# Performance work log

Measured on AMD Instinct MI355X. Metric: run time of the kernel, lower is better.

Reference implementation:

```python
import jax, jax.numpy as jnp
import numpy as np

EMBED_DIM = 1024
NUM_HEADS = 16
HEAD_DIM = EMBED_DIM // NUM_HEADS  # 64
B, NQ, NK = 4, 1024, 2048


def setup_inputs() -> dict:
    key = jax.random.key(0)
    ks = jax.random.split(key, 13)
    s = 1.0 / np.sqrt(EMBED_DIM)
    inp = {
        "query": jax.random.normal(ks[0], (B, NQ, EMBED_DIM), jnp.float32),
        "key": jax.random.normal(ks[1], (B, NK, EMBED_DIM), jnp.float32),
        "value": jax.random.normal(ks[2], (B, NK, EMBED_DIM), jnp.float32),
        # positive multiplicity weights per key element
        "key_multiplicities": jax.random.uniform(ks[3], (B, NK), jnp.float32, 0.1, 4.0),
        "wq_w": jax.random.normal(ks[4], (EMBED_DIM, EMBED_DIM), jnp.float32) * s,
        "wq_b": jnp.zeros((EMBED_DIM,), jnp.float32),
        "wk_w": jax.random.normal(ks[5], (EMBED_DIM, EMBED_DIM), jnp.float32) * s,
        "wk_b": jnp.zeros((EMBED_DIM,), jnp.float32),
        "wv_w": jax.random.normal(ks[6], (EMBED_DIM, EMBED_DIM), jnp.float32) * s,
        "wv_b": jnp.zeros((EMBED_DIM,), jnp.float32),
        "wo_w": jax.random.normal(ks[7], (EMBED_DIM, EMBED_DIM), jnp.float32) * s,
        "wo_b": jnp.zeros((EMBED_DIM,), jnp.float32),
    }
    return inp


def _split_heads(x, b, n):
    # (b, n, h*d) -> (b, h, n, d)
    return x.reshape(b, n, NUM_HEADS, HEAD_DIM).transpose(0, 2, 1, 3)


def reference(query, key, value, key_multiplicities,
              wq_w, wq_b, wk_w, wk_b, wv_w, wv_b, wo_w, wo_b):
    b, n_q, _ = query.shape
    _, n_k, _ = key.shape
    q = _split_heads(query @ wq_w.T + wq_b, b, n_q)   # (b, h, n_q, d)
    k = _split_heads(key @ wk_w.T + wk_b, b, n_k)     # (b, h, n_k, d)
    v = _split_heads(value @ wv_w.T + wv_b, b, n_k)   # (b, h, n_k, d)
    scale = 1.0 / jnp.sqrt(jnp.asarray(HEAD_DIM, q.dtype))
    scores = jnp.einsum("bhqd,bhkd->bhqk", q, k) * scale
    # multiplicities weight each key: softmax_i(m_i * exp(s_i)) == softmax(s_i + log m_i)
    logits = scores + jnp.log(key_multiplicities)[:, None, None, :]
    attn = jax.nn.softmax(logits, axis=-1)            # (b, h, n_q, n_k)
    out = jnp.einsum("bhqk,bhkd->bhqd", attn, v)
    out = out.transpose(0, 2, 1, 3).reshape(b, n_q, NUM_HEADS * HEAD_DIM)
    return out @ wo_w.T + wo_b
```

## Files before the change

kernel.cpp:

```cpp
#include <hip/hip_runtime.h>
#include <hip/hip_bf16.h>
#include <stdint.h>
#include <stddef.h>

typedef __attribute__((ext_vector_type(8))) short bf16x8;
typedef __attribute__((ext_vector_type(4))) short short4v;
typedef __attribute__((ext_vector_type(4))) float f32x4;
typedef __attribute__((ext_vector_type(2))) uint32_t u32x2;
typedef __attribute__((ext_vector_type(4))) uint32_t u32x4;

#define MFMA16(a, b, c) __builtin_amdgcn_mfma_f32_16x16x32_bf16((a), (b), (c), 0, 0, 0)

__device__ __forceinline__ short f2bf(float f) {
    uint32_t u = __builtin_bit_cast(uint32_t, f);
    u = (u + 0x7FFFu + ((u >> 16) & 1u)) >> 16;
    return (short)(uint16_t)u;
}

__device__ __forceinline__ uint32_t pkbf(float a, float b) {
#if __has_builtin(__builtin_amdgcn_cvt_pk_bf16_f32)
    auto r = __builtin_amdgcn_cvt_pk_bf16_f32(a, b);
    return __builtin_bit_cast(uint32_t, r);
#else
    return (uint32_t)(uint16_t)f2bf(a) | ((uint32_t)(uint16_t)f2bf(b) << 16);
#endif
}

__device__ __forceinline__ float fexp2(float x) {
#if __has_builtin(__builtin_amdgcn_exp2f)
    return __builtin_amdgcn_exp2f(x);
#else
    return exp2f(x);
#endif
}

__device__ __forceinline__ void gload16(const short* g, short* l) {
    __builtin_amdgcn_global_load_lds(
        (const __attribute__((address_space(1))) unsigned int*)g,
        (__attribute__((address_space(3))) unsigned int*)l, 16, 0, 0);
}

__global__ __launch_bounds__(256) void prep_kernel(
        const float* __restrict__ w0, const float* __restrict__ w1,
        const float* __restrict__ w2, const float* __restrict__ w3,
        const float* __restrict__ q, const float* __restrict__ k,
        const float* __restrict__ v, const float* __restrict__ m,
        short* __restrict__ wb, short* __restrict__ Qa,
        short* __restrict__ Ka, short* __restrict__ Va,
        float* __restrict__ lm) {
    const int bid = blockIdx.x;
    if (bid >= 12288) {
        const int i = ((bid - 12288) * 256 + threadIdx.x) * 8;
        f32x4 a = *(const f32x4*)(m + i);
        f32x4 b = *(const f32x4*)(m + i + 4);
        f32x4 oa, ob;
        #pragma unroll
        for (int j = 0; j < 4; ++j) { oa[j] = __log2f(a[j]); ob[j] = __log2f(b[j]); }
        *(f32x4*)(lm + i) = oa;
        *(f32x4*)(lm + i + 4) = ob;
        return;
    }
    const float* src;
    short* dst;
    int local;
    if (bid < 2048) {
        const int z = bid >> 9;
        local = bid & 511;
        src = (z == 0) ? w0 : (z == 1) ? w1 : (z == 2) ? w2 : w3;
        dst = wb + (size_t)z * 1048576;
    } else if (bid < 4096) { src = q; dst = Qa; local = bid - 2048; }
    else if (bid < 8192)   { src = k; dst = Ka; local = bid - 4096; }
    else                   { src = v; dst = Va; local = bid - 8192; }
    const size_t i = ((size_t)local * 256 + threadIdx.x) * 8;
    f32x4 a = *(const f32x4*)(src + i);
    f32x4 b = *(const f32x4*)(src + i + 4);
    u32x4 o = { pkbf(a[0], a[1]), pkbf(a[2], a[3]), pkbf(b[0], b[1]), pkbf(b[2], b[3]) };
    *(u32x4*)(dst + i) = o;
}

__global__ __launch_bounds__(256) void proj_kernel(
        const short* __restrict__ Qa, const short* __restrict__ Ka,
        const short* __restrict__ Va, const short* __restrict__ wb,
        const float* __restrict__ wq_b, const float* __restrict__ wk_b,
        const float* __restrict__ wv_b, short* __restrict__ Qp,
        short* __restrict__ Kp, short* __restrict__ Vt, const int ybase) {
    __shared__ short As[128 * 32];
    __shared__ short Bs[128 * 32];

    const int cpx = gridDim.x >> 3;
    const int l = (blockIdx.x & 7) * cpx + (blockIdx.x >> 3);
    const int y = (l >> 3) + ybase;
    const int tn = (l & 7) * 128;

    const short* A; const short* W; const float* bias; int mode, tm;
    if (y < 32)      { A = Qa; W = wb;           bias = wq_b; mode = 0; tm = y * 128; }
    else if (y < 96) { A = Ka; W = wb + 1048576; bias = wk_b; mode = 1; tm = (y - 32) * 128; }
    else             { A = Va; W = wb + 2097152; bias = wv_b; mode = 2; tm = (y - 96) * 128; }

    const int t = threadIdx.x, lane = t & 63, w = t >> 6;
    const int wr = w >> 1, wc = w & 1;
    const int qd = lane >> 4, c = lane & 15;

    f32x4 acc[4][4];
    #pragma unroll
    for (int i = 0; i < 4; ++i)
        #pragma unroll
        for (int j = 0; j < 4; ++j) acc[i][j] = (f32x4){0.f, 0.f, 0.f, 0.f};

    const int r0 = w * 16 + (lane >> 2);
    const int qc = (lane & 3) ^ ((lane >> 3) & 3);
    const short* ga0 = A + (size_t)(tm + r0) * 1024 + qc * 8;
    const short* ga1 = ga0 + 64 * 1024;
    const short* gb0 = W + (size_t)(tn + r0) * 1024 + qc * 8;
    const short* gb1 = gb0 + 64 * 1024;
    short* la0 = &As[w * 512];
    short* la1 = &As[w * 512 + 2048];
    short* lb0 = &Bs[w * 512];
    short* lb1 = &Bs[w * 512 + 2048];
    const int swz = (qd ^ ((c >> 1) & 3)) * 8;

    for (int k0 = 0; k0 < 1024; k0 += 32) {
        __syncthreads();
        gload16(ga0 + k0, la0);
        gload16(ga1 + k0, la1);
        gload16(gb0 + k0, lb0);
        gload16(gb1 + k0, lb1);
        __syncthreads();
        bf16x8 af[4], bfr[4];
        #pragma unroll
        for (int rt = 0; rt < 4; ++rt)
            af[rt] = *(const bf16x8*)&As[(wr * 64 + rt * 16 + c) * 32 + swz];
        #pragma unroll
        for (int ct = 0; ct < 4; ++ct)
            bfr[ct] = *(const bf16x8*)&Bs[(wc * 64 + ct * 16 + c) * 32 + swz];
        #pragma unroll
        for (int rt = 0; rt < 4; ++rt)
            #pragma unroll
            for (int ct = 0; ct < 4; ++ct)
                acc[rt][ct] = MFMA16(af[rt], bfr[ct], acc[rt][ct]);
    }

    float bv[4];
    #pragma unroll
    for (int ct = 0; ct < 4; ++ct) bv[ct] = bias[tn + wc * 64 + ct * 16 + c];

    if (mode == 2) {
        #pragma unroll
        for (int rt = 0; rt < 4; ++rt)
            #pragma unroll
            for (int ct = 0; ct < 4; ++ct) {
                const int cg = tn + wc * 64 + ct * 16 + c;
                const int h = cg >> 6, d = cg & 63;
                const int rg0 = tm + wr * 64 + rt * 16 + qd * 4;
                const int bb = rg0 >> 11, n = rg0 & 2047;
                u32x2 pk = { pkbf(acc[rt][ct][0] + bv[ct], acc[rt][ct][1] + bv[ct]),
                             pkbf(acc[rt][ct][2] + bv[ct], acc[rt][ct][3] + bv[ct]) };
                *(u32x2*)&Vt[((((size_t)(bb * 16 + h)) * 64 + d) << 11) + n] = pk;
            }
    } else {
        short* out = (mode == 0) ? Qp : Kp;
        const int nshift = (mode == 0) ? 10 : 11;
        const int mask = (1 << nshift) - 1;
        #pragma unroll
        for (int rt = 0; rt < 4; ++rt)
            #pragma unroll
            for (int ct = 0; ct < 4; ++ct) {
                const int cg = tn + wc * 64 + ct * 16 + c;
                const int h = cg >> 6, d = cg & 63;
                #pragma unroll
                for (int r = 0; r < 4; ++r) {
                    const int rg = tm + wr * 64 + rt * 16 + qd * 4 + r;
                    const int bb = rg >> nshift, n = rg & mask;
                    out[((((size_t)(bb * 16 + h)) << nshift) + n) * 64 + d] =
                        f2bf(acc[rt][ct][r] + bv[ct]);
                }
            }
    }
}

__global__ __launch_bounds__(256, 4) void gemm_o_kernel(
        const short* __restrict__ Ob, const short* __restrict__ W,
        const float* __restrict__ bias, float* __restrict__ out) {
    __shared__ short As[128 * 32];
    __shared__ short Bs[64 * 32];

    const int cpx = gridDim.x >> 3;
    const int l = (blockIdx.x & 7) * cpx + (blockIdx.x >> 3);
    const int tm = (l >> 4) * 128, tn = (l & 15) * 64;

    const int t = threadIdx.x, lane = t & 63, w = t >> 6;
    const int wr = w >> 1, wc = w & 1;
    const int qd = lane >> 4, c = lane & 15;

    f32x4 acc[4][2];
    #pragma unroll
    for (int i = 0; i < 4; ++i)
        #pragma unroll
        for (int j = 0; j < 2; ++j) acc[i][j] = (f32x4){0.f, 0.f, 0.f, 0.f};

    const int r0 = w * 16 + (lane >> 2);
    const int qc = (lane & 3) ^ ((lane >> 3) & 3);
    const short* ga0 = Ob + (size_t)(tm + r0) * 1024 + qc * 8;
    const short* ga1 = ga0 + 64 * 1024;
    const short* gb0 = W + (size_t)(tn + r0) * 1024 + qc * 8;
    short* la0 = &As[w * 512];
    short* la1 = &As[w * 512 + 2048];
    short* lb0 = &Bs[w * 512];
    const int swz = (qd ^ ((c >> 1) & 3)) * 8;

    for (int k0 = 0; k0 < 1024; k0 += 32) {
        __syncthreads();
        gload16(ga0 + k0, la0);
        gload16(ga1 + k0, la1);
        gload16(gb0 + k0, lb0);
        __syncthreads();
        bf16x8 af[4], bfr[2];
        #pragma unroll
        for (int rt = 0; rt < 4; ++rt)
            af[rt] = *(const bf16x8*)&As[(wr * 64 + rt * 16 + c) * 32 + swz];
        #pragma unroll
        for (int ct = 0; ct < 2; ++ct)
            bfr[ct] = *(const bf16x8*)&Bs[(wc * 32 + ct * 16 + c) * 32 + swz];
        #pragma unroll
        for (int rt = 0; rt < 4; ++rt)
            #pragma unroll
            for (int ct = 0; ct < 2; ++ct)
                acc[rt][ct] = MFMA16(af[rt], bfr[ct], acc[rt][ct]);
    }

    float bv[2];
    #pragma unroll
    for (int ct = 0; ct < 2; ++ct) bv[ct] = bias[tn + wc * 32 + ct * 16 + c];

    #pragma unroll
    for (int rt = 0; rt < 4; ++rt)
        #pragma unroll
        for (int ct = 0; ct < 2; ++ct) {
            const int cg = tn + wc * 32 + ct * 16 + c;
            #pragma unroll
            for (int r = 0; r < 4; ++r) {
                const int rg = tm + wr * 64 + rt * 16 + qd * 4 + r;
                out[(size_t)rg * 1024 + cg] = acc[rt][ct][r] + bv[ct];
            }
        }
}

__global__ __launch_bounds__(256, 2) void attn_kernel(
        const short* __restrict__ Qp, const short* __restrict__ Kp,
        const short* __restrict__ Vt, const float* __restrict__ logm,
        short* __restrict__ Ob) {
    __shared__ short Ps[128 * 128];
    __shared__ short Vs[64 * 128];
    __shared__ float Lm[128];
    short* Ks = Ps;

    const int bid = blockIdx.x;
    const int xcd = bid & 7, ii = bid >> 3;
    const int qt = ii >> 3, bh = xcd + ((ii & 7) << 3);
    const int b = bh >> 4;
    const int t = threadIdx.x, lane = t & 63, w = t >> 6;
    const int qd = lane >> 4, c = lane & 15;
    const int cl = c & 7;
    const float SC = 0.18033688011112042f;

    bf16x8 qf[2][2];
    #pragma unroll
    for (int ct = 0; ct < 2; ++ct)
        #pragma unroll
        for (int kd = 0; kd < 2; ++kd)
            qf[ct][kd] = *(const bf16x8*)(Qp +
                ((size_t)bh * 1024 + qt * 128 + w * 32 + ct * 16 + c) * 64 + kd * 32 + qd * 8);

    bf16x8 onesf;
    {
        const short ov = (c == 0) ? (short)0x3F80 : (short)0;
        #pragma unroll
        for (int j = 0; j < 8; ++j) onesf[j] = ov;
    }

    f32x4 oacc[2][5];
    #pragma unroll
    for (int i = 0; i < 2; ++i)
        #pragma unroll
        for (int j = 0; j < 5; ++j) oacc[i][j] = (f32x4){0.f, 0.f, 0.f, 0.f};

    const short* kgp[4];
    short* klp[4];
    const short* vgp[4];
    short* vlp[4];
    {
        const int krow = lane >> 3;
        const int kchk = (lane & 7) ^ krow;
        const int vrow = lane >> 4;
        #pragma unroll
        for (int i = 0; i < 4; ++i) {
            const int rk = w * 32 + i * 8 + krow;
            kgp[i] = Kp + ((size_t)bh * 2048 + rk) * 64 + kchk * 8;
            klp[i] = &Ks[(w * 4 + i) * 512];
            const int rv = w * 16 + i * 4 + vrow;
            const int vchk = (lane & 15) ^ (rv & 7);
            vgp[i] = Vt + ((size_t)bh * 64 + rv) * 2048 + vchk * 8;
            vlp[i] = &Vs[(w * 4 + i) * 512];
        }
    }

    for (int kt = 0; kt < 16; ++kt) {
        #pragma unroll
        for (int i = 0; i < 4; ++i) {
            gload16(kgp[i] + (size_t)kt * 8192, klp[i]);
            gload16(vgp[i] + kt * 128, vlp[i]);
        }
        if (t < 128) Lm[t] = logm[b * 2048 + kt * 128 + t];
        __syncthreads();

        f32x4 s[8][2];
        #pragma unroll
        for (int rt = 0; rt < 8; ++rt) {
            bf16x8 a0 = *(const bf16x8*)&Ks[(rt * 16 + c) * 64 + (qd ^ cl) * 8];
            bf16x8 a1 = *(const bf16x8*)&Ks[(rt * 16 + c) * 64 + ((4 | qd) ^ cl) * 8];
            #pragma unroll
            for (int ct = 0; ct < 2; ++ct) {
                f32x4 z = (f32x4){0.f, 0.f, 0.f, 0.f};
                s[rt][ct] = MFMA16(a1, qf[ct][1], MFMA16(a0, qf[ct][0], z));
            }
        }
        __syncthreads();

        #pragma unroll
        for (int rt = 0; rt < 8; ++rt) {
            f32x4 lv = *(const f32x4*)&Lm[rt * 16 + qd * 4];
            #pragma unroll
            for (int ct = 0; ct < 2; ++ct) {
                float p0 = fexp2(__builtin_fmaf(s[rt][ct][0], SC, lv[0]));
                float p1 = fexp2(__builtin_fmaf(s[rt][ct][1], SC, lv[1]));
                float p2 = fexp2(__builtin_fmaf(s[rt][ct][2], SC, lv[2]));
                float p3 = fexp2(__builtin_fmaf(s[rt][ct][3], SC, lv[3]));
                u32x2 pk = { pkbf(p0, p1), pkbf(p2, p3) };
                const int prow = w * 32 + ct * 16 + c;
                const int pch = (2 * rt + (qd >> 1)) ^ cl;
                *(u32x2*)&Ps[prow * 128 + pch * 8 + (qd & 1) * 4] = pk;
            }
        }

        #pragma unroll
        for (int kk = 0; kk < 4; ++kk) {
            const int lch = ((kk * 4 + qd) ^ cl) * 8;
            bf16x8 pf[2], vf[4];
            #pragma unroll
            for (int rtq = 0; rtq < 2; ++rtq)
                pf[rtq] = *(const bf16x8*)&Ps[(w * 32 + rtq * 16 + c) * 128 + lch];
            #pragma unroll
            for (int ct = 0; ct < 4; ++ct)
                vf[ct] = *(const bf16x8*)&Vs[(ct * 16 + c) * 128 + lch];
            #pragma unroll
            for (int rtq = 0; rtq < 2; ++rtq) {
                #pragma unroll
                for (int ct = 0; ct < 4; ++ct)
                    oacc[rtq][ct] = MFMA16(pf[rtq], vf[ct], oacc[rtq][ct]);
                oacc[rtq][4] = MFMA16(pf[rtq], onesf, oacc[rtq][4]);
            }
        }
        __syncthreads();
    }

    const int h = bh & 15;
    float inv[2][4];
    #pragma unroll
    for (int rtq = 0; rtq < 2; ++rtq)
        #pragma unroll
        for (int r = 0; r < 4; ++r)
            inv[rtq][r] = 1.f / __shfl(oacc[rtq][4][r], qd * 16);
    #pragma unroll
    for (int rtq = 0; rtq < 2; ++rtq)
        #pragma unroll
        for (int ct = 0; ct < 4; ++ct)
            #pragma unroll
            for (int r = 0; r < 4; ++r) {
                const int qg = qt * 128 + w * 32 + rtq * 16 + qd * 4 + r;
                const int e = h * 64 + ct * 16 + c;
                Ob[((size_t)(b * 1024 + qg)) * 1024 + e] = f2bf(oacc[rtq][ct][r] * inv[rtq][r]);
            }
}

extern "C" void kernel_launch(void* const* d_in, const int* in_sizes, int n_in,
                              void* d_out, int out_size, void* d_ws, size_t ws_size,
                              hipStream_t stream) {
    (void)in_sizes; (void)n_in; (void)out_size;
    const float* query = (const float*)d_in[0];
    const float* key   = (const float*)d_in[1];
    const float* value = (const float*)d_in[2];
    const float* mult  = (const float*)d_in[3];
    const float* wq_w  = (const float*)d_in[4];
    const float* wq_b  = (const float*)d_in[5];
    const float* wk_w  = (const float*)d_in[6];
    const float* wk_b  = (const float*)d_in[7];
    const float* wv_w  = (const float*)d_in[8];
    const float* wv_b  = (const float*)d_in[9];
    const float* wo_w  = (const float*)d_in[10];
    const float* wo_b  = (const float*)d_in[11];
    float* out = (float*)d_out;

    char* ws = (char*)d_ws;
    const size_t MB = 1024 * 1024;
    const bool merged = ws_size >= 89 * MB;

    short* wb = (short*)(ws + 0 * MB);
    short* Qa = (short*)(ws + 8 * MB);
    short* Ka = (short*)(ws + 16 * MB);
    short* Va = (short*)(ws + 32 * MB);
    short* Qp = (short*)(ws + 48 * MB);
    short* Kp = (short*)(ws + 56 * MB);
    short *Vt, *Ob; float* lm;
    if (merged) {
        Vt = (short*)(ws + 72 * MB);
        Ob = (short*)(ws + 8 * MB);
        lm = (float*)(ws + 88 * MB);
    } else {
        Vt = (short*)(ws + 8 * MB);
        Ob = (short*)(ws + 32 * MB);
        lm = (float*)(ws + 72 * MB);
    }

    prep_kernel<<<dim3(12292), 256, 0, stream>>>(
        wq_w, wk_w, wv_w, wo_w, query, key, value, mult, wb, Qa, Ka, Va, lm);
    if (merged) {
        proj_kernel<<<dim3(1280), 256, 0, stream>>>(
            Qa, Ka, Va, wb, wq_b, wk_b, wv_b, Qp, Kp, Vt, 0);
    } else {
        proj_kernel<<<dim3(768), 256, 0, stream>>>(
            Qa, Ka, Va, wb, wq_b, wk_b, wv_b, Qp, Kp, Vt, 0);
        proj_kernel<<<dim3(512), 256, 0, stream>>>(
            Qa, Ka, Va, wb, wq_b, wk_b, wv_b, Qp, Kp, Vt, 96);
    }
    attn_kernel<<<dim3(512), 256, 0, stream>>>(Qp, Kp, Vt, lm, Ob);
    gemm_o_kernel<<<dim3(512), 256, 0, stream>>>(Ob, wb + 3145728, wo_b, out);
}
```

Measured before the change: 285.8 us.

## Double-buffer LDS tiles in projection and output GEMM kernels

Adds two LDS buffers per operand in the QKV projection and output projection GEMMs. The global-to-LDS load of the next K-slice is issued before the MFMA work on the current slice, which halves the barriers per slice and hides load latency behind compute. The cost is doubled shared memory per block, which may lower occupancy, and correctness depends on gload16 being an asynchronous direct-to-LDS load that the following barrier waits on.

```diff
diff --git a/kernel.cpp b/kernel.cpp
--- a/kernel.cpp
+++ b/kernel.cpp
@@ -84,8 +84,8 @@
         const float* __restrict__ wq_b, const float* __restrict__ wk_b,
         const float* __restrict__ wv_b, short* __restrict__ Qp,
         short* __restrict__ Kp, short* __restrict__ Vt, const int ybase) {
-    __shared__ short As[128 * 32];
-    __shared__ short Bs[128 * 32];
+    __shared__ short As[2][128 * 32];
+    __shared__ short Bs[2][128 * 32];
 
     const int cpx = gridDim.x >> 3;
     const int l = (blockIdx.x & 7) * cpx + (blockIdx.x >> 3);
@@ -113,31 +113,40 @@
     const short* ga1 = ga0 + 64 * 1024;
     const short* gb0 = W + (size_t)(tn + r0) * 1024 + qc * 8;
     const short* gb1 = gb0 + 64 * 1024;
-    short* la0 = &As[w * 512];
-    short* la1 = &As[w * 512 + 2048];
-    short* lb0 = &Bs[w * 512];
-    short* lb1 = &Bs[w * 512 + 2048];
+    const int lofs = w * 512;
     const int swz = (qd ^ ((c >> 1) & 3)) * 8;
 
-    for (int k0 = 0; k0 < 1024; k0 += 32) {
-        __syncthreads();
-        gload16(ga0 + k0, la0);
-        gload16(ga1 + k0, la1);
-        gload16(gb0 + k0, lb0);
-        gload16(gb1 + k0, lb1);
-        __syncthreads();
+    auto stage = [&](int buf, int k0) {
+        gload16(ga0 + k0, &As[buf][lofs]);
+        gload16(ga1 + k0, &As[buf][lofs + 2048]);
+        gload16(gb0 + k0, &Bs[buf][lofs]);
+        gload16(gb1 + k0, &Bs[buf][lofs + 2048]);
+    };
+    auto compute = [&](const short* Ab, const short* Bb) {
         bf16x8 af[4], bfr[4];
         #pragma unroll
         for (int rt = 0; rt < 4; ++rt)
-            af[rt] = *(const bf16x8*)&As[(wr * 64 + rt * 16 + c) * 32 + swz];
+            af[rt] = *(const bf16x8*)&Ab[(wr * 64 + rt * 16 + c) * 32 + swz];
         #pragma unroll
         for (int ct = 0; ct < 4; ++ct)
-            bfr[ct] = *(const bf16x8*)&Bs[(wc * 64 + ct * 16 + c) * 32 + swz];
+            bfr[ct] = *(const bf16x8*)&Bb[(wc * 64 + ct * 16 + c) * 32 + swz];
         #pragma unroll
         for (int rt = 0; rt < 4; ++rt)
             #pragma unroll
             for (int ct = 0; ct < 4; ++ct)
                 acc[rt][ct] = MFMA16(af[rt], bfr[ct], acc[rt][ct]);
+    };
+
+    stage(0, 0);
+    __syncthreads();
+    for (int k0 = 0; k0 < 1024; k0 += 64) {
+        stage(1, k0 + 32);
+        compute(As[0], Bs[0]);
+        __syncthreads();
+        if (k0 + 64 < 1024)
+            stage(0, k0 + 64);
+        compute(As[1], Bs[1]);
+        __syncthreads();
     }
 
     float bv[4];
@@ -181,8 +190,8 @@
 __global__ __launch_bounds__(256, 4) void gemm_o_kernel(
         const short* __restrict__ Ob, const short* __restrict__ W,
         const float* __restrict__ bias, float* __restrict__ out) {
-    __shared__ short As[128 * 32];
-    __shared__ short Bs[64 * 32];
+    __shared__ short As[2][128 * 32];
+    __shared__ short Bs[2][64 * 32];
 
     const int cpx = gridDim.x >> 3;
     const int l = (blockIdx.x & 7) * cpx + (blockIdx.x >> 3);
@@ -203,29 +212,39 @@
     const short* ga0 = Ob + (size_t)(tm + r0) * 1024 + qc * 8;
     const short* ga1 = ga0 + 64 * 1024;
     const short* gb0 = W + (size_t)(tn + r0) * 1024 + qc * 8;
-    short* la0 = &As[w * 512];
-    short* la1 = &As[w * 512 + 2048];
-    short* lb0 = &Bs[w * 512];
+    const int lofs = w * 512;
     const int swz = (qd ^ ((c >> 1) & 3)) * 8;
 
-    for (int k0 = 0; k0 < 1024; k0 += 32) {
-        __syncthreads();
-        gload16(ga0 + k0, la0);
-        gload16(ga1 + k0, la1);
-        gload16(gb0 + k0, lb0);
-        __syncthreads();
+    auto stage = [&](int buf, int k0) {
+        gload16(ga0 + k0, &As[buf][lofs]);
+        gload16(ga1 + k0, &As[buf][lofs + 2048]);
+        gload16(gb0 + k0, &Bs[buf][lofs]);
+    };
+    auto compute = [&](const short* Ab, const short* Bb) {
         bf16x8 af[4], bfr[2];
         #pragma unroll
         for (int rt = 0; rt < 4; ++rt)
-            af[rt] = *(const bf16x8*)&As[(wr * 64 + rt * 16 + c) * 32 + swz];
+            af[rt] = *(const bf16x8*)&Ab[(wr * 64 + rt * 16 + c) * 32 + swz];
         #pragma unroll
         for (int ct = 0; ct < 2; ++ct)
-            bfr[ct] = *(const bf16x8*)&Bs[(wc * 32 + ct * 16 + c) * 32 + swz];
+            bfr[ct] = *(const bf16x8*)&Bb[(wc * 32 + ct * 16 + c) * 32 + swz];
         #pragma unroll
         for (int rt = 0; rt < 4; ++rt)
             #pragma unroll
             for (int ct = 0; ct < 2; ++ct)
                 acc[rt][ct] = MFMA16(af[rt], bfr[ct], acc[rt][ct]);
+    };
+
+    stage(0, 0);
+    __syncthreads();
+    for (int k0 = 0; k0 < 1024; k0 += 64) {
+        stage(1, k0 + 32);
+        compute(As[0], Bs[0]);
+        __syncthreads();
+        if (k0 + 64 < 1024)
+            stage(0, k0 + 64);
+        compute(As[1], Bs[1]);
+        __syncthreads();
     }
 
     float bv[2];
```

Result: slower. 298.2 us (+4.3%).
